# Kernel optimization log

Measured on AMD Instinct MI355X. Metric: run time of the kernel, lower is better.

The kernel has to match this reference:

```python
import jax, jax.numpy as jnp
import numpy as np

N, E, D, H = 4096, 131072, 256, 8
DH = D // H  # head dim = 32


def layer_norm(x, g, b, eps=1e-5):
    mu = jnp.mean(x, axis=-1, keepdims=True)
    var = jnp.var(x, axis=-1, keepdims=True)
    return (x - mu) * jax.lax.rsqrt(var + eps) * g + b


def mlp2(x, w1, b1, w2, b2):
    # Linear -> GELU(exact) -> Linear (dropout is identity at inference)
    return jax.nn.gelu(x @ w1 + b1, approximate=False) @ w2 + b2


def setup_inputs() -> dict:
    key = jax.random.key(0)
    ks = iter(jax.random.split(key, 32))
    s = 0.02
    d = {
        'x': jax.random.normal(next(ks), (N, D), jnp.float32),
        'edge_index': jax.random.randint(next(ks), (2, E), 0, N, jnp.int32),
        'edge_attr': jax.random.normal(next(ks), (E, D), jnp.float32),
        # GINE eps
        'eps': jnp.zeros((1,), jnp.float32),
        # edge MLP (Linear weights stored [in, out])
        'e_w1': jax.random.normal(next(ks), (D, D), jnp.float32) * s,
        'e_b1': jnp.zeros((D,), jnp.float32),
        'e_w2': jax.random.normal(next(ks), (D, D), jnp.float32) * s,
        'e_b2': jnp.zeros((D,), jnp.float32),
        # update MLP
        'u_w1': jax.random.normal(next(ks), (D, D), jnp.float32) * s,
        'u_b1': jnp.zeros((D,), jnp.float32),
        'u_w2': jax.random.normal(next(ks), (D, D), jnp.float32) * s,
        'u_b2': jnp.zeros((D,), jnp.float32),
        # LayerNorms
        'ln_local_g': jnp.ones((D,), jnp.float32), 'ln_local_b': jnp.zeros((D,), jnp.float32),
        'ln_global_g': jnp.ones((D,), jnp.float32), 'ln_global_b': jnp.zeros((D,), jnp.float32),
        'ln_ffn_g': jnp.ones((D,), jnp.float32), 'ln_ffn_b': jnp.zeros((D,), jnp.float32),
        # MHA projections ([in, out])
        'wq': jax.random.normal(next(ks), (D, D), jnp.float32) * s,
        'wk': jax.random.normal(next(ks), (D, D), jnp.float32) * s,
        'wv': jax.random.normal(next(ks), (D, D), jnp.float32) * s,
        'bq': jnp.zeros((D,), jnp.float32), 'bk': jnp.zeros((D,), jnp.float32), 'bv': jnp.zeros((D,), jnp.float32),
        'wo': jax.random.normal(next(ks), (D, D), jnp.float32) * s,
        'bo': jnp.zeros((D,), jnp.float32),
        # FFN
        'f_w1': jax.random.normal(next(ks), (D, 4 * D), jnp.float32) * s,
        'f_b1': jnp.zeros((4 * D,), jnp.float32),
        'f_w2': jax.random.normal(next(ks), (4 * D, D), jnp.float32) * s,
        'f_b2': jnp.zeros((D,), jnp.float32),
    }
    return d


def reference(x, edge_index, edge_attr, eps,
              e_w1, e_b1, e_w2, e_b2, u_w1, u_b1, u_w2, u_b2,
              ln_local_g, ln_local_b, ln_global_g, ln_global_b, ln_ffn_g, ln_ffn_b,
              wq, wk, wv, bq, bk, bv, wo, bo,
              f_w1, f_b1, f_w2, f_b2):
    src, dst = edge_index[0], edge_index[1]
    n = x.shape[0]

    # ---- local GINE conv on pre-normed features ----
    h = layer_norm(x, ln_local_g, ln_local_b)
    messages = mlp2(h[src] + edge_attr, e_w1, e_b1, e_w2, e_b2)  # [E, D]
    aggregated = jax.ops.segment_sum(messages, dst, num_segments=n)  # [N, D]
    local = mlp2((1.0 + eps) * h + aggregated, u_w1, u_b1, u_w2, u_b2)
    x = x + local

    # ---- global multihead self-attention over all nodes ----
    g = layer_norm(x, ln_global_g, ln_global_b)
    q = (g @ wq + bq).reshape(n, H, DH)
    k = (g @ wk + bk).reshape(n, H, DH)
    v = (g @ wv + bv).reshape(n, H, DH)
    scores = jnp.einsum('nhd,mhd->hnm', q, k) / jnp.sqrt(jnp.float32(DH))
    attn = jax.nn.softmax(scores, axis=-1)
    ctx = jnp.einsum('hnm,mhd->nhd', attn, v).reshape(n, D)
    x = x + (ctx @ wo + bo)

    # ---- FFN ----
    x = x + mlp2(layer_norm(x, ln_ffn_g, ln_ffn_b), f_w1, f_b1, f_w2, f_b2)
    return x
```

## Files before the change

### kernel.cpp

```cpp
#include <hip/hip_runtime.h>
#include <math.h>

#define N_NODES 4096
#define N_EDGES 131072
#define XPAD    272

using bf16x8 = __attribute__((ext_vector_type(8))) __bf16;
using f32x4  = __attribute__((ext_vector_type(4))) float;
typedef unsigned short u16;

__device__ __forceinline__ u16 f2bf(float f) {
  union { __bf16 b; u16 u; } cv; cv.b = (__bf16)f; return cv.u;
}
__device__ __forceinline__ float bf2f(u16 h) {
  return __uint_as_float(((unsigned)h) << 16);
}
__device__ __forceinline__ float gelu_tanh(float x) {
  float t = x * x;
  float y = x * (1.5957691216057308f + 0.07135481627f * t);
  float e = __expf(y);
  return x - x / (1.0f + e);
}
__device__ __forceinline__ f32x4 mfma16(bf16x8 a, bf16x8 b, f32x4 c) {
  return __builtin_amdgcn_mfma_f32_16x16x32_bf16(a, b, c, 0, 0, 0);
}

struct WPtrs { const float* p[10]; };
struct OPtrs { float* o[4]; float* l; };

__global__ void setup_kernel(WPtrs w, u16* __restrict__ dst, float qscale,
                             const int* __restrict__ ei, int* __restrict__ deg,
                             const float* __restrict__ bq, const float* __restrict__ bk,
                             const float* __restrict__ bv, float* __restrict__ qkvbias) {
  int blk = blockIdx.x, t = threadIdx.x;
  if (blk < 512) {
    int tid = blk * 256 + t;
    int m, ci;
    if (tid < 32768)      { m = tid >> 13;                 ci = tid & 8191; }
    else if (tid < 57344) { m = 4 + ((tid - 32768) >> 13); ci = (tid - 32768) & 8191; }
    else if (tid < 65536) { m = 7; ci = tid - 57344; }
    else if (tid < 98304) { m = 8; ci = tid - 65536; }
    else                  { m = 9; ci = tid - 98304; }
    int Cols = (m == 8) ? 1024 : 256;
    int k8   = (m == 8) ? (ci >> 10) : (ci >> 8);
    int c    = (m == 8) ? (ci & 1023) : (ci & 255);
    const float* src = w.p[m] + (size_t)(k8 * 8) * Cols + c;
    float sc = (m == 4) ? qscale : 1.0f;
    u16 tmp[8];
#pragma unroll
    for (int j = 0; j < 8; ++j) tmp[j] = f2bf(src[(size_t)j * Cols] * sc);
    size_t off;
    if (m < 4)       off = (size_t)(m << 16) + (size_t)(k8 * 256 + c) * 8;
    else if (m < 7)  off = 262144 + (size_t)(k8 * 768 + (m - 4) * 256 + c) * 8;
    else if (m == 7) off = 458752 + (size_t)(k8 * 256 + c) * 8;
    else if (m == 8) off = 524288 + (size_t)(k8 * 1024 + c) * 8;
    else             off = 786432 + (size_t)(k8 * 256 + c) * 8;
    *(uint4*)(dst + off) = *(const uint4*)tmp;
  } else if (blk < 1024) {
    int e = (blk - 512) * 256 + t;
    atomicAdd(&deg[ei[N_EDGES + e]], 1);
  } else {
#pragma unroll
    for (int i = 0; i < 3; ++i) {
      int idx = i * 256 + t;
      qkvbias[idx] = idx < 256 ? bq[idx] * qscale : (idx < 512 ? bk[idx - 256] : bv[idx - 512]);
    }
  }
}

__global__ void scan_kernel(const int* __restrict__ deg, int* __restrict__ offs) {
  __shared__ int part[1024];
  int t = threadIdx.x;
  int base = t * 4;
  int a0 = deg[base], a1 = deg[base + 1], a2 = deg[base + 2], a3 = deg[base + 3];
  int s = a0 + a1 + a2 + a3;
  part[t] = s;
  __syncthreads();
  for (int off = 1; off < 1024; off <<= 1) {
    int v = (t >= off) ? part[t - off] : 0;
    __syncthreads();
    part[t] += v;
    __syncthreads();
  }
  int excl = part[t] - s;
  offs[base] = excl;
  offs[base + 1] = excl + a0;
  offs[base + 2] = excl + a0 + a1;
  offs[base + 3] = excl + a0 + a1 + a2;
  if (t == 1023) offs[4096] = part[1023];
}

__global__ void mid_kernel(const int* __restrict__ ei, const int* __restrict__ offs,
                           int* __restrict__ cnt, int* __restrict__ eperm,
                           int* __restrict__ dst_s, int* __restrict__ src_s,
                           const float* __restrict__ x, const float* __restrict__ g,
                           const float* __restrict__ b, float* __restrict__ hf,
                           u16* __restrict__ hb) {
  int blk = blockIdx.x, t = threadIdx.x;
  if (blk < 512) {
    int e = blk * 256 + t;
    int d = ei[N_EDGES + e];
    int p = offs[d] + atomicAdd(&cnt[d], 1);
    eperm[p] = e;
    dst_s[p] = d;
    src_s[p] = ei[e];
  } else {
    int row = blk - 512;
    float v = x[(size_t)row * 256 + t];
    float s1 = v, s2 = v * v;
#pragma unroll
    for (int o = 32; o > 0; o >>= 1) { s1 += __shfl_xor(s1, o); s2 += __shfl_xor(s2, o); }
    __shared__ float a1[4], a2[4];
    int wv = t >> 6, lane = t & 63;
    if (lane == 0) { a1[wv] = s1; a2[wv] = s2; }
    __syncthreads();
    s1 = a1[0] + a1[1] + a1[2] + a1[3];
    s2 = a2[0] + a2[1] + a2[2] + a2[3];
    float mean = s1 * (1.0f / 256.0f);
    float var  = s2 * (1.0f / 256.0f) - mean * mean;
    float rs = rsqrtf(var + 1e-5f);
    float o = (v - mean) * rs * g[t] + b[t];
    hf[(size_t)row * 256 + t] = o;
    hb[(size_t)row * 256 + t] = f2bf(o);
  }
}

__launch_bounds__(512, 4)
__global__ void edge_kernel(const u16* __restrict__ hb, const float* __restrict__ ea,
                            const int* __restrict__ eperm, const int* __restrict__ src_s,
                            const int* __restrict__ dst_s, const int* __restrict__ offs,
                            const u16* __restrict__ wp1, const float* __restrict__ b1,
                            const u16* __restrict__ wp2, const float* __restrict__ b2,
                            float* __restrict__ agg) {
  __shared__ __align__(16) u16 X[128 * XPAD];
  __shared__ int gstart[130];
  __shared__ unsigned long long bm[2];
  __shared__ int Gs;
  const f32x4 fzero = {0.f, 0.f, 0.f, 0.f};
  int t = threadIdx.x;
  int lane = t & 63, wv = t >> 6;
  int lr = lane & 15, lq = lane >> 4;
  int wr = wv >> 2, wc = wv & 3;
  int e0 = blockIdx.x * 128;
  int col0 = wc * 64;
  int row0 = wr * 64;

  const u16* b1ptr = wp1 + ((size_t)lq * 256 + col0 + lr) * 8;
  const u16* b2ptr = wp2 + ((size_t)lq * 256 + col0 + lr) * 8;
  bf16x8 bc[4], bn[4];
#pragma unroll
  for (int ct = 0; ct < 4; ++ct) bc[ct] = *(const bf16x8*)(b1ptr + ct * 128);

  int ci = (t & 31) * 8;
#pragma unroll
  for (int it = 0; it < 8; ++it) {
    int r = it * 16 + (t >> 5);
    int e = eperm[e0 + r];
    int s = src_s[e0 + r];
    const float* pa = ea + (size_t)e * 256 + ci;
    float4 a0 = *(const float4*)pa;
    float4 a1 = *(const float4*)(pa + 4);
    ushort4 h0 = *(const ushort4*)(hb + (size_t)s * 256 + ci);
    ushort4 h1 = *(const ushort4*)(hb + (size_t)s * 256 + ci + 4);
    u16 tmp[8];
    tmp[0] = f2bf(a0.x + bf2f(h0.x)); tmp[1] = f2bf(a0.y + bf2f(h0.y));
    tmp[2] = f2bf(a0.z + bf2f(h0.z)); tmp[3] = f2bf(a0.w + bf2f(h0.w));
    tmp[4] = f2bf(a1.x + bf2f(h1.x)); tmp[5] = f2bf(a1.y + bf2f(h1.y));
    tmp[6] = f2bf(a1.z + bf2f(h1.z)); tmp[7] = f2bf(a1.w + bf2f(h1.w));
    *(uint4*)&X[r * XPAD + ci] = *(const uint4*)tmp;
  }
  int flag = 0;
  if (t < 128) {
    int d  = dst_s[e0 + t];
    int dp = (t == 0) ? -1 : dst_s[e0 + t - 1];
    flag = (d != dp) ? 1 : 0;
  }
  unsigned long long m = __ballot(flag);
  if (wv < 2 && lane == 0) bm[wv] = m;
  __syncthreads();

  f32x4 acc[4][4];
#pragma unroll
  for (int i = 0; i < 4; ++i)
#pragma unroll
    for (int j = 0; j < 4; ++j) acc[i][j] = fzero;

#pragma unroll
  for (int ks = 0; ks < 8; ++ks) {
    if (ks < 7) {
#pragma unroll
      for (int ct = 0; ct < 4; ++ct)
        bn[ct] = *(const bf16x8*)(b1ptr + (size_t)(ks + 1) * 8192 + ct * 128);
    }
    bf16x8 a[4];
#pragma unroll
    for (int rt = 0; rt < 4; ++rt)
      a[rt] = *(const bf16x8*)&X[(row0 + rt * 16 + lr) * XPAD + ks * 32 + lq * 8];
#pragma unroll
    for (int ct = 0; ct < 4; ++ct)
#pragma unroll
      for (int rt = 0; rt < 4; ++rt) acc[rt][ct] = mfma16(a[rt], bc[ct], acc[rt][ct]);
#pragma unroll
    for (int ct = 0; ct < 4; ++ct) bc[ct] = bn[ct];
  }
#pragma unroll
  for (int ct = 0; ct < 4; ++ct) bn[ct] = *(const bf16x8*)(b2ptr + ct * 128);
  if (t < 128 && flag) {
    int idx = __popcll(bm[wv] & ((1ull << lane) - 1));
    if (wv == 1) idx += __popcll(bm[0]);
    gstart[idx] = t;
  }
  if (t == 0) {
    int g = __popcll(bm[0]) + __popcll(bm[1]);
    Gs = g;
    gstart[g] = 128;
  }
  __syncthreads();

#pragma unroll
  for (int ct = 0; ct < 4; ++ct) {
    int c = col0 + ct * 16 + lr;
    float bb = b1[c];
#pragma unroll
    for (int rt = 0; rt < 4; ++rt)
#pragma unroll
      for (int r = 0; r < 4; ++r) {
        int row = row0 + rt * 16 + lq * 4 + r;
        X[row * XPAD + c] = f2bf(gelu_tanh(acc[rt][ct][r] + bb));
      }
  }
#pragma unroll
  for (int ct = 0; ct < 4; ++ct) bc[ct] = bn[ct];
  __syncthreads();

#pragma unroll
  for (int i = 0; i < 4; ++i)
#pragma unroll
    for (int j = 0; j < 4; ++j) acc[i][j] = fzero;
#pragma unroll
  for (int ks = 0; ks < 8; ++ks) {
    if (ks < 7) {
#pragma unroll
      for (int ct = 0; ct < 4; ++ct)
        bn[ct] = *(const bf16x8*)(b2ptr + (size_t)(ks + 1) * 8192 + ct * 128);
    }
    bf16x8 a[4];
#pragma unroll
    for (int rt = 0; rt < 4; ++rt)
      a[rt] = *(const bf16x8*)&X[(row0 + rt * 16 + lr) * XPAD + ks * 32 + lq * 8];
#pragma unroll
    for (int ct = 0; ct < 4; ++ct)
#pragma unroll
      for (int rt = 0; rt < 4; ++rt) acc[rt][ct] = mfma16(a[rt], bc[ct], acc[rt][ct]);
#pragma unroll
    for (int ct = 0; ct < 4; ++ct) bc[ct] = bn[ct];
  }
  __syncthreads();

#pragma unroll
  for (int ct = 0; ct < 4; ++ct) {
    int c = col0 + ct * 16 + lr;
    float bb = b2[c];
#pragma unroll
    for (int rt = 0; rt < 4; ++rt)
#pragma unroll
      for (int r = 0; r < 4; ++r) {
        int row = row0 + rt * 16 + lq * 4 + r;
        X[row * XPAD + c] = f2bf(acc[rt][ct][r] + bb);
      }
  }
  __syncthreads();

  {
    int G = Gs;
    int c4 = lane * 4;
    for (int gi = wv; gi < G; gi += 8) {
      int rs = gstart[gi], re = gstart[gi + 1];
      int d = dst_s[e0 + rs];
      float run0 = 0.f, run1 = 0.f, run2 = 0.f, run3 = 0.f;
      for (int r = rs; r < re; ++r) {
        ushort4 xv = *(const ushort4*)&X[r * XPAD + c4];
        run0 += bf2f(xv.x); run1 += bf2f(xv.y); run2 += bf2f(xv.z); run3 += bf2f(xv.w);
      }
      bool full = (offs[d] == e0 + rs) && (offs[d + 1] == e0 + re);
      float* p = &agg[(size_t)d * 256 + c4];
      if (full) {
        *(float4*)p = make_float4(run0, run1, run2, run3);
      } else {
        atomicAdd(p + 0, run0); atomicAdd(p + 1, run1);
        atomicAdd(p + 2, run2); atomicAdd(p + 3, run3);
      }
    }
  }
}

__launch_bounds__(256, 2)
__global__ void update_kernel(const float* __restrict__ hf, const float* __restrict__ agg,
                              const float* __restrict__ epsp, const float* __restrict__ xin,
                              const u16* __restrict__ wp1, const float* __restrict__ b1,
                              const u16* __restrict__ wp2, const float* __restrict__ b2,
                              const float* __restrict__ lng, const float* __restrict__ lnb,
                              float* __restrict__ x1, u16* __restrict__ gb) {
  __shared__ __align__(16) u16 X[64 * XPAD];
  __shared__ float S1[64][4], S2[64][4], MUs[64], RSs[64];
  const f32x4 fzero = {0.f, 0.f, 0.f, 0.f};
  int t = threadIdx.x;
  int lane = t & 63, wv = t >> 6;
  int lr = lane & 15, lq = lane >> 4;
  int n0 = blockIdx.x * 64;
  int col0 = wv * 64;
  float epv = 1.0f + epsp[0];
  const u16* b1ptr = wp1 + ((size_t)lq * 256 + col0 + lr) * 8;
  const u16* b2ptr = wp2 + ((size_t)lq * 256 + col0 + lr) * 8;
  bf16x8 bc[4], bn[4];
#pragma unroll
  for (int ct = 0; ct < 4; ++ct) bc[ct] = *(const bf16x8*)(b1ptr + ct * 128);
  {
    int c4 = (t & 63) * 4;
#pragma unroll
    for (int ii = 0; ii < 16; ++ii) {
      int r = ii * 4 + wv;
      float4 h = *(const float4*)(hf + (size_t)(n0 + r) * 256 + c4);
      float4 a = *(const float4*)(agg + (size_t)(n0 + r) * 256 + c4);
      *(ushort4*)&X[r * XPAD + c4] =
          make_ushort4(f2bf(epv * h.x + a.x), f2bf(epv * h.y + a.y),
                       f2bf(epv * h.z + a.z), f2bf(epv * h.w + a.w));
    }
  }
  __syncthreads();
  f32x4 acc[4][4];
#pragma unroll
  for (int i = 0; i < 4; ++i)
#pragma unroll
    for (int j = 0; j < 4; ++j) acc[i][j] = fzero;
#pragma unroll
  for (int ks = 0; ks < 8; ++ks) {
    if (ks < 7) {
#pragma unroll
      for (int ct = 0; ct < 4; ++ct)
        bn[ct] = *(const bf16x8*)(b1ptr + (size_t)(ks + 1) * 8192 + ct * 128);
    }
    bf16x8 a[4];
#pragma unroll
    for (int rt = 0; rt < 4; ++rt)
      a[rt] = *(const bf16x8*)&X[(rt * 16 + lr) * XPAD + ks * 32 + lq * 8];
#pragma unroll
    for (int ct = 0; ct < 4; ++ct)
#pragma unroll
      for (int rt = 0; rt < 4; ++rt) acc[rt][ct] = mfma16(a[rt], bc[ct], acc[rt][ct]);
#pragma unroll
    for (int ct = 0; ct < 4; ++ct) bc[ct] = bn[ct];
  }
#pragma unroll
  for (int ct = 0; ct < 4; ++ct) bn[ct] = *(const bf16x8*)(b2ptr + ct * 128);
  __syncthreads();
#pragma unroll
  for (int ct = 0; ct < 4; ++ct) {
    int c = col0 + ct * 16 + lr;
    float bb = b1[c];
#pragma unroll
    for (int rt = 0; rt < 4; ++rt)
#pragma unroll
      for (int r = 0; r < 4; ++r) {
        int row = rt * 16 + lq * 4 + r;
        X[row * XPAD + c] = f2bf(gelu_tanh(acc[rt][ct][r] + bb));
      }
  }
#pragma unroll
  for (int ct = 0; ct < 4; ++ct) bc[ct] = bn[ct];
  __syncthreads();
#pragma unroll
  for (int i = 0; i < 4; ++i)
#pragma unroll
    for (int j = 0; j < 4; ++j) acc[i][j] = fzero;
#pragma unroll
  for (int ks = 0; ks < 8; ++ks) {
    if (ks < 7) {
#pragma unroll
      for (int ct = 0; ct < 4; ++ct)
        bn[ct] = *(const bf16x8*)(b2ptr + (size_t)(ks + 1) * 8192 + ct * 128);
    }
    bf16x8 a[4];
#pragma unroll
    for (int rt = 0; rt < 4; ++rt)
      a[rt] = *(const bf16x8*)&X[(rt * 16 + lr) * XPAD + ks * 32 + lq * 8];
#pragma unroll
    for (int ct = 0; ct < 4; ++ct)
#pragma unroll
      for (int rt = 0; rt < 4; ++rt) acc[rt][ct] = mfma16(a[rt], bc[ct], acc[rt][ct]);
#pragma unroll
    for (int ct = 0; ct < 4; ++ct) bc[ct] = bn[ct];
  }
  float bb2[4];
#pragma unroll
  for (int ct = 0; ct < 4; ++ct) bb2[ct] = b2[col0 + ct * 16 + lr];
#pragma unroll
  for (int rt = 0; rt < 4; ++rt)
#pragma unroll
    for (int r = 0; r < 4; ++r) {
      int row = rt * 16 + lq * 4 + r;
      int grow = n0 + row;
      float p1 = 0.f, p2 = 0.f;
#pragma unroll
      for (int ct = 0; ct < 4; ++ct) {
        int c = col0 + ct * 16 + lr;
        float v = acc[rt][ct][r] + bb2[ct] + xin[(size_t)grow * 256 + c];
        x1[(size_t)grow * 256 + c] = v;
        acc[rt][ct][r] = v;
        p1 += v; p2 += v * v;
      }
#pragma unroll
      for (int o = 1; o < 16; o <<= 1) { p1 += __shfl_xor(p1, o); p2 += __shfl_xor(p2, o); }
      if (lr == 0) { S1[row][wv] = p1; S2[row][wv] = p2; }
    }
  __syncthreads();
  if (t < 64) {
    float s1 = S1[t][0] + S1[t][1] + S1[t][2] + S1[t][3];
    float s2 = S2[t][0] + S2[t][1] + S2[t][2] + S2[t][3];
    float mu = s1 * (1.0f / 256.0f);
    float var = s2 * (1.0f / 256.0f) - mu * mu;
    MUs[t] = mu;
    RSs[t] = rsqrtf(var + 1e-5f);
  }
  __syncthreads();
  float gv[4], bv[4];
#pragma unroll
  for (int ct = 0; ct < 4; ++ct) {
    int c = col0 + ct * 16 + lr;
    gv[ct] = lng[c]; bv[ct] = lnb[c];
  }
#pragma unroll
  for (int rt = 0; rt < 4; ++rt)
#pragma unroll
    for (int r = 0; r < 4; ++r) {
      int row = rt * 16 + lq * 4 + r;
      int grow = n0 + row;
      float mu = MUs[row], rs = RSs[row];
#pragma unroll
      for (int ct = 0; ct < 4; ++ct) {
        int c = col0 + ct * 16 + lr;
        gb[(size_t)grow * 256 + c] = f2bf((acc[rt][ct][r] - mu) * rs * gv[ct] + bv[ct]);
      }
    }
}

template <int ROWS, bool GELU_F, bool RES, bool OUTB, bool LNF, bool QKV>
__launch_bounds__(256, 2)
__global__ void gemm_kernel(const u16* __restrict__ A, int lda,
                            const u16* __restrict__ Wp, int K, int WCols,
                            const float* __restrict__ bias, float scale,
                            const float* __restrict__ res,
                            const float* __restrict__ lng, const float* __restrict__ lnb,
                            float* __restrict__ outf, u16* __restrict__ outh,
                            u16* __restrict__ outh2, u16* __restrict__ vtp, int ldo) {
  __shared__ __align__(16) u16 X[ROWS * XPAD];
  __shared__ float S1[LNF ? ROWS : 1][4], S2[LNF ? ROWS : 1][4];
  __shared__ float MUs[LNF ? ROWS : 1], RSs[LNF ? ROWS : 1];
  constexpr int RT = ROWS / 16;
  const f32x4 fzero = {0.f, 0.f, 0.f, 0.f};
  int t = threadIdx.x;
  int lane = t & 63, wv = t >> 6;
  int lr = lane & 15, lq = lane >> 4;
  int r0 = blockIdx.x * ROWS;
  int cb = blockIdx.y * 256;
  f32x4 acc[RT][4];
#pragma unroll
  for (int i = 0; i < RT; ++i)
#pragma unroll
    for (int j = 0; j < 4; ++j) acc[i][j] = fzero;
  const u16* bptr = Wp + ((size_t)lq * WCols + cb + wv * 64 + lr) * 8;
  bf16x8 bc[4], bn[4];
#pragma unroll
  for (int ct = 0; ct < 4; ++ct) bc[ct] = *(const bf16x8*)(bptr + ct * 128);
  int rr = t >> 5, c8 = (t & 31) * 8;
  for (int kc = 0; kc < K; kc += 256) {
#pragma unroll
    for (int ii = 0; ii < ROWS / 8; ++ii) {
      int r = ii * 8 + rr;
      *(uint4*)&X[r * XPAD + c8] = *(const uint4*)(A + (size_t)(r0 + r) * lda + kc + c8);
    }
    __syncthreads();
#pragma unroll
    for (int ks = 0; ks < 8; ++ks) {
      bool more = (ks < 7) || (kc + 256 < K);
      if (more) {
        size_t koff = (ks < 7) ? ((size_t)(kc >> 3) + (ks + 1) * 4) * WCols
                               : ((size_t)((kc + 256) >> 3)) * WCols;
#pragma unroll
        for (int ct = 0; ct < 4; ++ct)
          bn[ct] = *(const bf16x8*)(bptr + (koff + ct * 16) * 8);
      }
      bf16x8 a[RT];
#pragma unroll
      for (int rt = 0; rt < RT; ++rt)
        a[rt] = *(const bf16x8*)&X[(rt * 16 + lr) * XPAD + ks * 32 + lq * 8];
#pragma unroll
      for (int ct = 0; ct < 4; ++ct)
#pragma unroll
        for (int rt = 0; rt < RT; ++rt) acc[rt][ct] = mfma16(a[rt], bc[ct], acc[rt][ct]);
#pragma unroll
      for (int ct = 0; ct < 4; ++ct) bc[ct] = bn[ct];
    }
    __syncthreads();
  }
  if (QKV) {
    int y = blockIdx.y;
#pragma unroll
    for (int ct = 0; ct < 4; ++ct) {
      int c = cb + wv * 64 + ct * 16 + lr;
      float bb = bias[c];
#pragma unroll
      for (int rt = 0; rt < RT; ++rt)
#pragma unroll
        for (int r = 0; r < 4; ++r) {
          int row = r0 + rt * 16 + lq * 4 + r;
          u16 hv = f2bf(acc[rt][ct][r] + bb);
          if (y == 0)      outh[(size_t)row * 256 + c] = hv;
          else if (y == 1) outh2[(size_t)row * 256 + (c - 256)] = hv;
          else             vtp[(size_t)(c - 512) * 4096 + row] = hv;
        }
    }
  } else if (!LNF) {
#pragma unroll
    for (int ct = 0; ct < 4; ++ct) {
      int c = cb + wv * 64 + ct * 16 + lr;
      float bb = bias[c];
#pragma unroll
      for (int rt = 0; rt < RT; ++rt)
#pragma unroll
        for (int r = 0; r < 4; ++r) {
          int row = r0 + rt * 16 + lq * 4 + r;
          float v = (acc[rt][ct][r] + bb) * scale;
          if (GELU_F) v = gelu_tanh(v);
          if (RES) v += res[(size_t)row * 256 + c];
          if (OUTB) outh[(size_t)row * ldo + c] = f2bf(v);
          else      outf[(size_t)row * ldo + c] = v;
        }
    }
  } else {
    float bb[4];
#pragma unroll
    for (int ct = 0; ct < 4; ++ct) bb[ct] = bias[wv * 64 + ct * 16 + lr];
#pragma unroll
    for (int rt = 0; rt < RT; ++rt)
#pragma unroll
      for (int r = 0; r < 4; ++r) {
        int row = rt * 16 + lq * 4 + r;
        int grow = r0 + row;
        float p1 = 0.f, p2 = 0.f;
#pragma unroll
        for (int ct = 0; ct < 4; ++ct) {
          int c = wv * 64 + ct * 16 + lr;
          float v = acc[rt][ct][r] + bb[ct];
          if (RES) v += res[(size_t)grow * 256 + c];
          outf[(size_t)grow * 256 + c] = v;
          acc[rt][ct][r] = v;
          p1 += v; p2 += v * v;
        }
#pragma unroll
        for (int o = 1; o < 16; o <<= 1) { p1 += __shfl_xor(p1, o); p2 += __shfl_xor(p2, o); }
        if (lr == 0) { S1[row][wv] = p1; S2[row][wv] = p2; }
      }
    __syncthreads();
    if (t < ROWS) {
      float s1 = S1[t][0] + S1[t][1] + S1[t][2] + S1[t][3];
      float s2 = S2[t][0] + S2[t][1] + S2[t][2] + S2[t][3];
      float mu = s1 * (1.0f / 256.0f);
      float var = s2 * (1.0f / 256.0f) - mu * mu;
      MUs[t] = mu;
      RSs[t] = rsqrtf(var + 1e-5f);
    }
    __syncthreads();
    float gv[4], bv[4];
#pragma unroll
    for (int ct = 0; ct < 4; ++ct) {
      int c = wv * 64 + ct * 16 + lr;
      gv[ct] = lng[c]; bv[ct] = lnb[c];
    }
#pragma unroll
    for (int rt = 0; rt < RT; ++rt)
#pragma unroll
      for (int r = 0; r < 4; ++r) {
        int row = rt * 16 + lq * 4 + r;
        int grow = r0 + row;
        float mu = MUs[row], rs = RSs[row];
#pragma unroll
        for (int ct = 0; ct < 4; ++ct) {
          int c = wv * 64 + ct * 16 + lr;
          outh[(size_t)grow * ldo + c] = f2bf((acc[rt][ct][r] - mu) * rs * gv[ct] + bv[ct]);
        }
      }
  }
}

__launch_bounds__(256, 6)
__global__ void attn_kernel(const u16* __restrict__ qb, const u16* __restrict__ kb,
                            const u16* __restrict__ vT, OPtrs op) {
  __shared__ u16 Kt[64 * 40];
  __shared__ u16 Vt[32 * 72];
  __shared__ float P32[4][1024];
  const f32x4 fzero = {0.f, 0.f, 0.f, 0.f};
  int t = threadIdx.x;
  int lane = t & 63, wv = t >> 6;
  int lr = lane & 15, lq = lane >> 4;
  int head = blockIdx.y;
  int z = blockIdx.z;
  int q0 = blockIdx.x * 64 + wv * 16;
  int kbase = z * 1024;
  bf16x8 qf = *(const bf16x8*)(qb + (size_t)(q0 + lr) * 256 + head * 32 + lq * 8);
  f32x4 o0 = fzero, o1 = fzero;
  float l_i[4] = {0.f, 0.f, 0.f, 0.f};
  int kkey = t >> 2, kdp = (t & 3) * 8;
  int vd = t >> 3, vkc = (t & 7) * 8;
  const u16* vbase = vT + (size_t)(head * 32 + vd) * 4096;
  int psw = (lr >> 2) & 3;
  float* pw = &P32[wv][0];
  uint4 kreg = *(const uint4*)(kb + (size_t)(kbase + kkey) * 256 + head * 32 + kdp);
  uint4 vreg = *(const uint4*)(vbase + kbase + vkc);
  for (int it = 0; it < 16; ++it) {
    __syncthreads();
    *(uint4*)&Kt[kkey * 40 + kdp] = kreg;
    *(uint4*)&Vt[vd * 72 + vkc]   = vreg;
    if (it < 15) {
      int kn = kbase + (it + 1) * 64;
      kreg = *(const uint4*)(kb + (size_t)(kn + kkey) * 256 + head * 32 + kdp);
      vreg = *(const uint4*)(vbase + kn + vkc);
    }
    __syncthreads();
    f32x4 s[4];
#pragma unroll
    for (int ct = 0; ct < 4; ++ct) {
      bf16x8 bk = *(const bf16x8*)&Kt[(ct * 16 + lr) * 40 + lq * 8];
      s[ct] = mfma16(qf, bk, fzero);
    }
#pragma unroll
    for (int ct = 0; ct < 4; ++ct)
#pragma unroll
      for (int r = 0; r < 4; ++r) s[ct][r] = __expf(s[ct][r]);
#pragma unroll
    for (int r = 0; r < 4; ++r) {
      float ps = (s[0][r] + s[1][r]) + (s[2][r] + s[3][r]);
#pragma unroll
      for (int d = 1; d < 16; d <<= 1) ps += __shfl_xor(ps, d);
      l_i[r] += ps;
    }
#pragma unroll
    for (int ct = 0; ct < 4; ++ct) {
      int col = ct * 16 + lr;
      int w = (((col >> 2) ^ lq) << 2) + (col & 3);
#pragma unroll
      for (int r = 0; r < 4; ++r) pw[(lq * 4 + r) * 64 + w] = s[ct][r];
    }
#pragma unroll
    for (int kp = 0; kp < 2; ++kp) {
      int cch = kp * 8 + lq * 2;
      f32x4 f0 = *(const f32x4*)&pw[lr * 64 + ((cch ^ psw) << 2)];
      f32x4 f1 = *(const f32x4*)&pw[lr * 64 + (((cch + 1) ^ psw) << 2)];
      bf16x8 pa;
#pragma unroll
      for (int j = 0; j < 4; ++j) { pa[j] = (__bf16)f0[j]; pa[j + 4] = (__bf16)f1[j]; }
      bf16x8 v0 = *(const bf16x8*)&Vt[lr * 72 + kp * 32 + lq * 8];
      bf16x8 v1 = *(const bf16x8*)&Vt[(16 + lr) * 72 + kp * 32 + lq * 8];
      o0 = mfma16(pa, v0, o0);
      o1 = mfma16(pa, v1, o1);
    }
  }
  float* ob = op.o[z];
  float* lp = op.l + z * 32768;
#pragma unroll
  for (int r = 0; r < 4; ++r) {
    int row = q0 + lq * 4 + r;
    ob[(size_t)row * 256 + head * 32 + lr]      = o0[r];
    ob[(size_t)row * 256 + head * 32 + 16 + lr] = o1[r];
    if (lr == 0) lp[row * 8 + head] = l_i[r];
  }
}

__global__ void attn_merge(OPtrs op, u16* __restrict__ ctx) {
  int c = threadIdx.x;
  int head = c >> 5;
#pragma unroll
  for (int r = 0; r < 4; ++r) {
    int row = blockIdx.x * 4 + r;
    size_t idx = (size_t)row * 256 + c;
    float o = op.o[0][idx] + op.o[1][idx] + op.o[2][idx] + op.o[3][idx];
    int li = row * 8 + head;
    float l = op.l[li] + op.l[32768 + li] + op.l[65536 + li] + op.l[98304 + li];
    ctx[idx] = f2bf(o / l);
  }
}

extern "C" void kernel_launch(void* const* d_in, const int* in_sizes, int n_in,
                              void* d_out, int out_size, void* d_ws, size_t ws_size,
                              hipStream_t stream) {
  const float* x         = (const float*)d_in[0];
  const int*   ei        = (const int*)d_in[1];
  const float* edge_attr = (const float*)d_in[2];
  const float* eps       = (const float*)d_in[3];
  const float* e_w1 = (const float*)d_in[4];
  const float* e_b1 = (const float*)d_in[5];
  const float* e_w2 = (const float*)d_in[6];
  const float* e_b2 = (const float*)d_in[7];
  const float* u_w1 = (const float*)d_in[8];
  const float* u_b1 = (const float*)d_in[9];
  const float* u_w2 = (const float*)d_in[10];
  const float* u_b2 = (const float*)d_in[11];
  const float* ln_local_g  = (const float*)d_in[12];
  const float* ln_local_b  = (const float*)d_in[13];
  const float* ln_global_g = (const float*)d_in[14];
  const float* ln_global_b = (const float*)d_in[15];
  const float* ln_ffn_g    = (const float*)d_in[16];
  const float* ln_ffn_b    = (const float*)d_in[17];
  const float* wq = (const float*)d_in[18];
  const float* wk = (const float*)d_in[19];
  const float* wv = (const float*)d_in[20];
  const float* bq = (const float*)d_in[21];
  const float* bk = (const float*)d_in[22];
  const float* bv = (const float*)d_in[23];
  const float* wo = (const float*)d_in[24];
  const float* bo = (const float*)d_in[25];
  const float* f_w1 = (const float*)d_in[26];
  const float* f_b1 = (const float*)d_in[27];
  const float* f_w2 = (const float*)d_in[28];
  const float* f_b2 = (const float*)d_in[29];

  char* ws = (char*)d_ws;
  u16*   WP      = (u16*)(ws + 0);
  float* agg     = (float*)(ws + (2u  << 20));
  int*   deg     = (int*)(ws + (6u  << 20));
  int*   cnt     = (int*)(ws + (6u  << 20) + (16u << 10));
  int*   offs    = (int*)(ws + (6u  << 20) + (32u << 10));
  float* qkvbias = (float*)(ws + (6u << 20) + (64u << 10));
  float* hf      = (float*)(ws + (7u  << 20));
  float* x1      = (float*)(ws + (11u << 20));
  u16*   gb      = (u16*)(ws + (15u << 20));
  u16*   qbuf    = (u16*)(ws + (17u << 20));
  u16*   kbuf    = (u16*)(ws + (19u << 20));
  u16*   vTb     = (u16*)(ws + (21u << 20));
  u16*   ctxb    = (u16*)(ws + (23u << 20));
  float* x2      = (float*)(ws + (25u << 20));
  u16*   yb      = (u16*)(ws + (29u << 20));
  u16*   hid     = (u16*)(ws + (31u << 20));
  int*   eperm   = (int*)(ws + (39u << 20));
  int*   dst_s   = (int*)(ws + (39u << 20) + (512u << 10));
  int*   src_s   = (int*)(ws + (40u << 20));
  u16*   hb      = (u16*)(ws + (40u << 20) + (512u << 10));

  const size_t O_EW1 = 0, O_EW2 = 65536, O_UW1 = 131072, O_UW2 = 196608,
               O_QKV = 262144, O_WO = 458752, O_FW1 = 524288, O_FW2 = 786432;
  const float qscale = 0.17677669529663687f;

  hipMemsetAsync(agg, 0, (4u << 20) + (32u << 10), stream);

  WPtrs wp;
  wp.p[0] = e_w1; wp.p[1] = e_w2; wp.p[2] = u_w1; wp.p[3] = u_w2;
  wp.p[4] = wq;   wp.p[5] = wk;   wp.p[6] = wv;   wp.p[7] = wo;
  wp.p[8] = f_w1; wp.p[9] = f_w2;
  setup_kernel<<<1025, 256, 0, stream>>>(wp, WP, qscale, ei, deg, bq, bk, bv, qkvbias);
  scan_kernel<<<1, 1024, 0, stream>>>(deg, offs);
  mid_kernel<<<4608, 256, 0, stream>>>(ei, offs, cnt, eperm, dst_s, src_s,
                                       x, ln_local_g, ln_local_b, hf, hb);

  edge_kernel<<<N_EDGES / 128, 512, 0, stream>>>(hb, edge_attr, eperm, src_s, dst_s, offs,
                                                 WP + O_EW1, e_b1, WP + O_EW2, e_b2, agg);

  update_kernel<<<N_NODES / 64, 256, 0, stream>>>(hf, agg, eps, x,
                                                  WP + O_UW1, u_b1, WP + O_UW2, u_b2,
                                                  ln_global_g, ln_global_b, x1, gb);

  gemm_kernel<64, false, false, true, false, true><<<dim3(64, 3), 256, 0, stream>>>(
      gb, 256, WP + O_QKV, 256, 768, qkvbias, 1.0f, nullptr, nullptr, nullptr,
      nullptr, qbuf, kbuf, vTb, 256);

  OPtrs op;
  op.o[0] = agg;
  op.o[1] = hf;
  op.o[2] = x2;
  op.o[3] = (float*)(ws + (31u << 20));
  op.l    = (float*)(ws + (29u << 20));
  attn_kernel<<<dim3(64, 8, 4), 256, 0, stream>>>(qbuf, kbuf, vTb, op);
  attn_merge<<<N_NODES / 4, 256, 0, stream>>>(op, ctxb);

  gemm_kernel<32, false, true, false, true, false><<<dim3(128, 1), 256, 0, stream>>>(
      ctxb, 256, WP + O_WO, 256, 256, bo, 1.0f, x1, ln_ffn_g, ln_ffn_b, x2, yb,
      nullptr, nullptr, 256);

  gemm_kernel<64, true, false, true, false, false><<<dim3(64, 4), 256, 0, stream>>>(
      yb, 256, WP + O_FW1, 256, 1024, f_b1, 1.0f, nullptr, nullptr, nullptr,
      nullptr, hid, nullptr, nullptr, 1024);

  gemm_kernel<32, false, true, false, false, false><<<dim3(128, 1), 256, 0, stream>>>(
      hid, 1024, WP + O_FW2, 1024, 256, f_b2, 1.0f, x2, nullptr, nullptr,
      (float*)d_out, nullptr, nullptr, nullptr, 256);
}
```

Measured before the change: 510.9 us.

## Make edge kernel persistent over four tiles with register-prefetched next-tile gather

Each edge block now processes four 128-edge tiles in sequence. While the MFMA GEMMs for the current tile run, the gathered edge_attr and h[src] values for the next tile are prefetched into registers, so global gather latency overlaps compute. This needs 48 extra VGPRs per thread for the prefetch buffers, so launch bounds drop from 4 to 2 blocks per CU. The grid shrinks from 1024 to 256 blocks, which reduces latency hiding from concurrent blocks and may leave CUs underused.

```diff
diff --git a/kernel.cpp b/kernel.cpp
--- a/kernel.cpp
+++ b/kernel.cpp
@@ -125,7 +125,8 @@
   }
 }
 
-__launch_bounds__(512, 4)
+#define EK_NT 4
+__launch_bounds__(512, 2)
 __global__ void edge_kernel(const u16* __restrict__ hb, const float* __restrict__ ea,
                             const int* __restrict__ eperm, const int* __restrict__ src_s,
                             const int* __restrict__ dst_s, const int* __restrict__ offs,
@@ -141,155 +142,197 @@
   int lane = t & 63, wv = t >> 6;
   int lr = lane & 15, lq = lane >> 4;
   int wr = wv >> 2, wc = wv & 3;
-  int e0 = blockIdx.x * 128;
   int col0 = wc * 64;
   int row0 = wr * 64;
+  int tb = blockIdx.x * EK_NT;
 
   const u16* b1ptr = wp1 + ((size_t)lq * 256 + col0 + lr) * 8;
   const u16* b2ptr = wp2 + ((size_t)lq * 256 + col0 + lr) * 8;
+
+  int ci = (t & 31) * 8;
+  int rr5 = t >> 5;
+
+  float4 ra0[8], ra1[8];
+  ushort4 rh0[8], rh1[8];
+
+  auto LOADT = [&](int tile) {
+    int e0 = (tb + tile) * 128;
+#pragma unroll
+    for (int it = 0; it < 8; ++it) {
+      int r = it * 16 + rr5;
+      int e = eperm[e0 + r];
+      int s = src_s[e0 + r];
+      const float* pa = ea + (size_t)e * 256 + ci;
+      ra0[it] = *(const float4*)pa;
+      ra1[it] = *(const float4*)(pa + 4);
+      rh0[it] = *(const ushort4*)(hb + (size_t)s * 256 + ci);
+      rh1[it] = *(const ushort4*)(hb + (size_t)s * 256 + ci + 4);
+    }
+  };
+  auto WRITET = [&]() {
+#pragma unroll
+    for (int it = 0; it < 8; ++it) {
+      int r = it * 16 + rr5;
+      u16 tmp[8];
+      tmp[0] = f2bf(ra0[it].x + bf2f(rh0[it].x));
+      tmp[1] = f2bf(ra0[it].y + bf2f(rh0[it].y));
+      tmp[2] = f2bf(ra0[it].z + bf2f(rh0[it].z));
+      tmp[3] = f2bf(ra0[it].w + bf2f(rh0[it].w));
+      tmp[4] = f2bf(ra1[it].x + bf2f(rh1[it].x));
+      tmp[5] = f2bf(ra1[it].y + bf2f(rh1[it].y));
+      tmp[6] = f2bf(ra1[it].z + bf2f(rh1[it].z));
+      tmp[7] = f2bf(ra1[it].w + bf2f(rh1[it].w));
+      *(uint4*)&X[r * XPAD + ci] = *(const uint4*)tmp;
+    }
+  };
+
+  int flbits = 0;
+  if (t < 128) {
+#pragma unroll
+    for (int tt = 0; tt < EK_NT; ++tt) {
+      int e0 = (tb + tt) * 128;
+      int d  = dst_s[e0 + t];
+      int dp = (t == 0) ? -1 : dst_s[e0 + t - 1];
+      if (d != dp) flbits |= (1 << tt);
+    }
+  }
+
+  LOADT(0);
+  {
+    unsigned long long m = __ballot(flbits & 1);
+    if (wv < 2 && lane == 0) bm[wv] = m;
+  }
+  WRITET();
+  __syncthreads();
+
   bf16x8 bc[4], bn[4];
-#pragma unroll
-  for (int ct = 0; ct < 4; ++ct) bc[ct] = *(const bf16x8*)(b1ptr + ct * 128);
-
-  int ci = (t & 31) * 8;
-#pragma unroll
-  for (int it = 0; it < 8; ++it) {
-    int r = it * 16 + (t >> 5);
-    int e = eperm[e0 + r];
-    int s = src_s[e0 + r];
-    const float* pa = ea + (size_t)e * 256 + ci;
-    float4 a0 = *(const float4*)pa;
-    float4 a1 = *(const float4*)(pa + 4);
-    ushort4 h0 = *(const ushort4*)(hb + (size_t)s * 256 + ci);
-    ushort4 h1 = *(const ushort4*)(hb + (size_t)s * 256 + ci + 4);
-    u16 tmp[8];
-    tmp[0] = f2bf(a0.x + bf2f(h0.x)); tmp[1] = f2bf(a0.y + bf2f(h0.y));
-    tmp[2] = f2bf(a0.z + bf2f(h0.z)); tmp[3] = f2bf(a0.w + bf2f(h0.w));
-    tmp[4] = f2bf(a1.x + bf2f(h1.x)); tmp[5] = f2bf(a1.y + bf2f(h1.y));
-    tmp[6] = f2bf(a1.z + bf2f(h1.z)); tmp[7] = f2bf(a1.w + bf2f(h1.w));
-    *(uint4*)&X[r * XPAD + ci] = *(const uint4*)tmp;
-  }
-  int flag = 0;
-  if (t < 128) {
-    int d  = dst_s[e0 + t];
-    int dp = (t == 0) ? -1 : dst_s[e0 + t - 1];
-    flag = (d != dp) ? 1 : 0;
-  }
-  unsigned long long m = __ballot(flag);
-  if (wv < 2 && lane == 0) bm[wv] = m;
-  __syncthreads();
-
   f32x4 acc[4][4];
-#pragma unroll
-  for (int i = 0; i < 4; ++i)
-#pragma unroll
-    for (int j = 0; j < 4; ++j) acc[i][j] = fzero;
-
-#pragma unroll
-  for (int ks = 0; ks < 8; ++ks) {
-    if (ks < 7) {
+
+  for (int tt = 0; tt < EK_NT; ++tt) {
+    if (tt + 1 < EK_NT) LOADT(tt + 1);
+
+#pragma unroll
+    for (int ct = 0; ct < 4; ++ct) bc[ct] = *(const bf16x8*)(b1ptr + ct * 128);
+#pragma unroll
+    for (int i = 0; i < 4; ++i)
+#pragma unroll
+      for (int j = 0; j < 4; ++j) acc[i][j] = fzero;
+
+#pragma unroll
+    for (int ks = 0; ks < 8; ++ks) {
+      if (ks < 7) {
+#pragma unroll
+        for (int ct = 0; ct < 4; ++ct)
+          bn[ct] = *(const bf16x8*)(b1ptr + (size_t)(ks + 1) * 8192 + ct * 128);
+      }
+      bf16x8 a[4];
+#pragma unroll
+      for (int rt = 0; rt < 4; ++rt)
+        a[rt] = *(const bf16x8*)&X[(row0 + rt * 16 + lr) * XPAD + ks * 32 + lq * 8];
 #pragma unroll
       for (int ct = 0; ct < 4; ++ct)
-        bn[ct] = *(const bf16x8*)(b1ptr + (size_t)(ks + 1) * 8192 + ct * 128);
-    }
-    bf16x8 a[4];
-#pragma unroll
-    for (int rt = 0; rt < 4; ++rt)
-      a[rt] = *(const bf16x8*)&X[(row0 + rt * 16 + lr) * XPAD + ks * 32 + lq * 8];
-#pragma unroll
-    for (int ct = 0; ct < 4; ++ct)
-#pragma unroll
-      for (int rt = 0; rt < 4; ++rt) acc[rt][ct] = mfma16(a[rt], bc[ct], acc[rt][ct]);
+#pragma unroll
+        for (int rt = 0; rt < 4; ++rt) acc[rt][ct] = mfma16(a[rt], bc[ct], acc[rt][ct]);
+#pragma unroll
+      for (int ct = 0; ct < 4; ++ct) bc[ct] = bn[ct];
+    }
+#pragma unroll
+    for (int ct = 0; ct < 4; ++ct) bn[ct] = *(const bf16x8*)(b2ptr + ct * 128);
+    if (t < 128 && ((flbits >> tt) & 1)) {
+      int idx = __popcll(bm[wv] & ((1ull << lane) - 1));
+      if (wv == 1) idx += __popcll(bm[0]);
+      gstart[idx] = t;
+    }
+    if (t == 0) {
+      int g = __popcll(bm[0]) + __popcll(bm[1]);
+      Gs = g;
+      gstart[g] = 128;
+    }
+    __syncthreads();
+
+#pragma unroll
+    for (int ct = 0; ct < 4; ++ct) {
+      int c = col0 + ct * 16 + lr;
+      float bb = b1[c];
+#pragma unroll
+      for (int rt = 0; rt < 4; ++rt)
+#pragma unroll
+        for (int r = 0; r < 4; ++r) {
+          int row = row0 + rt * 16 + lq * 4 + r;
+          X[row * XPAD + c] = f2bf(gelu_tanh(acc[rt][ct][r] + bb));
+        }
+    }
 #pragma unroll
     for (int ct = 0; ct < 4; ++ct) bc[ct] = bn[ct];
-  }
-#pragma unroll
-  for (int ct = 0; ct < 4; ++ct) bn[ct] = *(const bf16x8*)(b2ptr + ct * 128);
-  if (t < 128 && flag) {
-    int idx = __popcll(bm[wv] & ((1ull << lane) - 1));
-    if (wv == 1) idx += __popcll(bm[0]);
-    gstart[idx] = t;
-  }
-  if (t == 0) {
-    int g = __popcll(bm[0]) + __popcll(bm[1]);
-    Gs = g;
-    gstart[g] = 128;
-  }
-  __syncthreads();
-
-#pragma unroll
-  for (int ct = 0; ct < 4; ++ct) {
-    int c = col0 + ct * 16 + lr;
-    float bb = b1[c];
-#pragma unroll
-    for (int rt = 0; rt < 4; ++rt)
-#pragma unroll
-      for (int r = 0; r < 4; ++r) {
-        int row = row0 + rt * 16 + lq * 4 + r;
-        X[row * XPAD + c] = f2bf(gelu_tanh(acc[rt][ct][r] + bb));
+    __syncthreads();
+
+#pragma unroll
+    for (int i = 0; i < 4; ++i)
+#pragma unroll
+      for (int j = 0; j < 4; ++j) acc[i][j] = fzero;
+#pragma unroll
+    for (int ks = 0; ks < 8; ++ks) {
+      if (ks < 7) {
+#pragma unroll
+        for (int ct = 0; ct < 4; ++ct)
+          bn[ct] = *(const bf16x8*)(b2ptr + (size_t)(ks + 1) * 8192 + ct * 128);
       }
-  }
-#pragma unroll
-  for (int ct = 0; ct < 4; ++ct) bc[ct] = bn[ct];
-  __syncthreads();
-
-#pragma unroll
-  for (int i = 0; i < 4; ++i)
-#pragma unroll
-    for (int j = 0; j < 4; ++j) acc[i][j] = fzero;
-#pragma unroll
-  for (int ks = 0; ks < 8; ++ks) {
-    if (ks < 7) {
+      bf16x8 a[4];
+#pragma unroll
+      for (int rt = 0; rt < 4; ++rt)
+        a[rt] = *(const bf16x8*)&X[(row0 + rt * 16 + lr) * XPAD + ks * 32 + lq * 8];
 #pragma unroll
       for (int ct = 0; ct < 4; ++ct)
-        bn[ct] = *(const bf16x8*)(b2ptr + (size_t)(ks + 1) * 8192 + ct * 128);
-    }
-    bf16x8 a[4];
-#pragma unroll
-    for (int rt = 0; rt < 4; ++rt)
-      a[rt] = *(const bf16x8*)&X[(row0 + rt * 16 + lr) * XPAD + ks * 32 + lq * 8];
-#pragma unroll
-    for (int ct = 0; ct < 4; ++ct)
-#pragma unroll
-      for (int rt = 0; rt < 4; ++rt) acc[rt][ct] = mfma16(a[rt], bc[ct], acc[rt][ct]);
-#pragma unroll
-    for (int ct = 0; ct < 4; ++ct) bc[ct] = bn[ct];
-  }
-  __syncthreads();
-
-#pragma unroll
-  for (int ct = 0; ct < 4; ++ct) {
-    int c = col0 + ct * 16 + lr;
-    float bb = b2[c];
-#pragma unroll
-    for (int rt = 0; rt < 4; ++rt)
-#pragma unroll
-      for (int r = 0; r < 4; ++r) {
-        int row = row0 + rt * 16 + lq * 4 + r;
-        X[row * XPAD + c] = f2bf(acc[rt][ct][r] + bb);
+#pragma unroll
+        for (int rt = 0; rt < 4; ++rt) acc[rt][ct] = mfma16(a[rt], bc[ct], acc[rt][ct]);
+#pragma unroll
+      for (int ct = 0; ct < 4; ++ct) bc[ct] = bn[ct];
+    }
+    __syncthreads();
+
+#pragma unroll
+    for (int ct = 0; ct < 4; ++ct) {
+      int c = col0 + ct * 16 + lr;
+      float bb = b2[c];
+#pragma unroll
+      for (int rt = 0; rt < 4; ++rt)
+#pragma unroll
+        for (int r = 0; r < 4; ++r) {
+          int row = row0 + rt * 16 + lq * 4 + r;
+          X[row * XPAD + c] = f2bf(acc[rt][ct][r] + bb);
+        }
+    }
+    __syncthreads();
+
+    {
+      int e0 = (tb + tt) * 128;
+      int G = Gs;
+      int c4 = lane * 4;
+      for (int gi = wv; gi < G; gi += 8) {
+        int rs = gstart[gi], re = gstart[gi + 1];
+        int d = dst_s[e0 + rs];
+        float run0 = 0.f, run1 = 0.f, run2 = 0.f, run3 = 0.f;
+        for (int r = rs; r < re; ++r) {
+          ushort4 xv = *(const ushort4*)&X[r * XPAD + c4];
+          run0 += bf2f(xv.x); run1 += bf2f(xv.y); run2 += bf2f(xv.z); run3 += bf2f(xv.w);
+        }
+        bool full = (offs[d] == e0 + rs) && (offs[d + 1] == e0 + re);
+        float* p = &agg[(size_t)d * 256 + c4];
+        if (full) {
+          *(float4*)p = make_float4(run0, run1, run2, run3);
+        } else {
+          atomicAdd(p + 0, run0); atomicAdd(p + 1, run1);
+          atomicAdd(p + 2, run2); atomicAdd(p + 3, run3);
+        }
       }
-  }
-  __syncthreads();
-
-  {
-    int G = Gs;
-    int c4 = lane * 4;
-    for (int gi = wv; gi < G; gi += 8) {
-      int rs = gstart[gi], re = gstart[gi + 1];
-      int d = dst_s[e0 + rs];
-      float run0 = 0.f, run1 = 0.f, run2 = 0.f, run3 = 0.f;
-      for (int r = rs; r < re; ++r) {
-        ushort4 xv = *(const ushort4*)&X[r * XPAD + c4];
-        run0 += bf2f(xv.x); run1 += bf2f(xv.y); run2 += bf2f(xv.z); run3 += bf2f(xv.w);
-      }
-      bool full = (offs[d] == e0 + rs) && (offs[d + 1] == e0 + re);
-      float* p = &agg[(size_t)d * 256 + c4];
-      if (full) {
-        *(float4*)p = make_float4(run0, run1, run2, run3);
-      } else {
-        atomicAdd(p + 0, run0); atomicAdd(p + 1, run1);
-        atomicAdd(p + 2, run2); atomicAdd(p + 3, run3);
-      }
+    }
+
+    if (tt + 1 < EK_NT) {
+      __syncthreads();
+      unsigned long long m = __ballot((flbits >> (tt + 1)) & 1);
+      if (wv < 2 && lane == 0) bm[wv] = m;
+      WRITET();
+      __syncthreads();
     }
   }
 }
@@ -761,8 +804,9 @@
   mid_kernel<<<4608, 256, 0, stream>>>(ei, offs, cnt, eperm, dst_s, src_s,
                                        x, ln_local_g, ln_local_b, hf, hb);
 
-  edge_kernel<<<N_EDGES / 128, 512, 0, stream>>>(hb, edge_attr, eperm, src_s, dst_s, offs,
-                                                 WP + O_EW1, e_b1, WP + O_EW2, e_b2, agg);
+  edge_kernel<<<N_EDGES / (128 * EK_NT), 512, 0, stream>>>(
+      hb, edge_attr, eperm, src_s, dst_s, offs,
+      WP + O_EW1, e_b1, WP + O_EW2, e_b2, agg);
 
   update_kernel<<<N_NODES / 64, 256, 0, stream>>>(hf, agg, eps, x,
                                                   WP + O_UW1, u_b1, WP + O_UW2, u_b2,
```

Result: slower. 644.0 us (+26.1%).
